# Kernel optimization log

Measured on AMD Instinct MI355X. Metric: run time of the kernel, lower is better.

The kernel has to match this reference:

```python
import jax, jax.numpy as jnp
import numpy as np

N_NODES = 50000
N_EDGES = 1600000
D_FEAT = 32
SCALE = 1.0
EPS = 1e-12


def setup_inputs() -> dict:
    key = jax.random.key(0)
    k1, k2 = jax.random.split(key)
    x = jax.random.normal(k1, (N_NODES, D_FEAT), dtype=jnp.float32)
    edge_index = jax.random.randint(k2, (2, N_EDGES), 0, N_NODES, dtype=jnp.int32)
    return {"x": x, "edge_index": edge_index}


def reference(x, edge_index):
    index_i = edge_index[0]  # target nodes (segments)
    index_j = edge_index[1]  # source nodes (gathered)

    # in-degree per target node, clamped to 1 (torch_scatter 'mean' semantics:
    # empty segments get mean 0)
    ones = jnp.ones((index_i.shape[0],), dtype=x.dtype)
    deg = jax.ops.segment_sum(ones, index_i, num_segments=N_NODES)
    deg = jnp.maximum(deg, 1.0)[:, None]  # [N, 1]

    # neighborhood mean of features
    mean = jax.ops.segment_sum(x[index_j], index_i, num_segments=N_NODES) / deg

    # neighborhood mean of squared deviations -> std
    reduced_x = (x - mean) ** 2
    var = jax.ops.segment_sum(reduced_x[index_j], index_i, num_segments=N_NODES) / deg
    std = jnp.sqrt(var + EPS)

    out = SCALE * x / std
    # replace infs with the original x, as in the torch module
    out = jnp.where(jnp.isinf(out), x, out)
    return out
```

## Files before the change

### kernel.cpp

```cpp
#include <hip/hip_runtime.h>
#include <hip/hip_fp16.h>
#include <math.h>

#define DF 32
#define EPSF 1e-12f
#define PB 128
#define PB_SHIFT 7
#define NBMAX 512
#define CAP 5120
#define CHUNK 4096
#define EPT 16

__global__ __launch_bounds__(256) void k_passA(
    const int* __restrict__ ii, const int* __restrict__ jj,
    const float* __restrict__ x, int* __restrict__ gcount,
    unsigned int* __restrict__ bucketed, __half* __restrict__ xh,
    int ne, int nb, int nfeat) {
  __shared__ int hist[NBMAX];
  __shared__ int histc[NBMAX];
  __shared__ int bb[NBMAX];
  __shared__ int excl_s[NBMAX];
  __shared__ int sc[256];
  __shared__ unsigned int stage[CHUNK];
  int t = threadIdx.x;
  hist[t] = 0; hist[t + 256] = 0;
  __syncthreads();

  int base = blockIdx.x * CHUNK;
  unsigned int pk[EPT];
  int rk[EPT];
#pragma unroll
  for (int k = 0; k < EPT; ++k) {
    int e = base + t + k * 256;
    if (e < ne) {
      int i = ii[e], j = jj[e];
      int b = i >> PB_SHIFT;
      pk[k] = ((unsigned)b << 23) | ((unsigned)(i & (PB - 1)) << 16) | (unsigned)j;
      rk[k] = atomicAdd(&hist[b], 1);
    } else {
      rk[k] = -1;
    }
  }

  {
    int base8 = blockIdx.x * (CHUNK / 8);
#pragma unroll
    for (int r = 0; r < 2; ++r) {
      int p8 = base8 + r * 256 + t;
      if (p8 * 8 < nfeat) {
        float4 a = ((const float4*)x)[2 * p8];
        float4 bq = ((const float4*)x)[2 * p8 + 1];
        union { __half2 h[4]; float4 f; } u;
        u.h[0] = __floats2half2_rn(a.x, a.y);
        u.h[1] = __floats2half2_rn(a.z, a.w);
        u.h[2] = __floats2half2_rn(bq.x, bq.y);
        u.h[3] = __floats2half2_rn(bq.z, bq.w);
        ((float4*)xh)[p8] = u.f;
      }
    }
  }
  __syncthreads();
  histc[t] = hist[t]; histc[t + 256] = hist[t + 256];
  __syncthreads();
#pragma unroll
  for (int b = t; b < NBMAX; b += 256) {
    int c = histc[b];
    bb[b] = (b < nb && c > 0) ? atomicAdd(&gcount[b], c) : 0;
  }
  int a0 = histc[2 * t], a1 = histc[2 * t + 1];
  sc[t] = a0 + a1;
  __syncthreads();
  int pv = sc[t];
  for (int s = 1; s < 256; s <<= 1) {
    int v = 0;
    if (t >= s) v = sc[t - s];
    __syncthreads();
    if (t >= s) sc[t] += v;
    __syncthreads();
  }
  int eP = sc[t] - pv;
  excl_s[2 * t] = eP;
  excl_s[2 * t + 1] = eP + a0;
  __syncthreads();
#pragma unroll
  for (int k = 0; k < EPT; ++k) {
    if (rk[k] >= 0) {
      int b = pk[k] >> 23;
      stage[excl_s[b] + rk[k]] = pk[k];
    }
  }
  __syncthreads();
  int bcnt = ne - base;
  if (bcnt > CHUNK) bcnt = CHUNK;
  for (int p = t; p < bcnt; p += 256) {
    unsigned int v = stage[p];
    int b = v >> 23;
    bucketed[(size_t)b * CAP + bb[b] + (p - excl_s[b])] = v;
  }
}

__global__ __launch_bounds__(256) void k_passB(
    const unsigned int* __restrict__ bucketed, const int* __restrict__ gcount,
    int* __restrict__ sortedj, int* __restrict__ deg_g, int* __restrict__ curend_g,
    int* __restrict__ perm, int n_nodes, int nb) {
  __shared__ int sc[256];
  __shared__ int lh[PB];
  __shared__ int lcur[PB];
  __shared__ int dh[PB];
  __shared__ int dcur[PB];
  __shared__ int sgbase;
  int b = blockIdx.x;
  int t = threadIdx.x;

  int g0 = (2 * t < nb) ? gcount[2 * t] : 0;
  int g1 = (2 * t + 1 < nb) ? gcount[2 * t + 1] : 0;
  sc[t] = g0 + g1;
  __syncthreads();
  int pv = sc[t];
  for (int s = 1; s < 256; s <<= 1) {
    int v = 0;
    if (t >= s) v = sc[t - s];
    __syncthreads();
    if (t >= s) sc[t] += v;
    __syncthreads();
  }
  if (2 * t == b) sgbase = sc[t] - pv;
  if (2 * t + 1 == b) sgbase = sc[t] - pv + g0;
  if (t < PB) { lh[t] = 0; dh[t] = 0; }
  __syncthreads();
  int gbase = sgbase;
  int cnt = gcount[b];

  const unsigned int* src = bucketed + (size_t)b * CAP;
  for (int p = t; p < cnt; p += 256) {
    int il = (src[p] >> 16) & (PB - 1);
    atomicAdd(&lh[il], 1);
  }
  __syncthreads();
  int a = (t < PB) ? lh[t] : 0;
  if (t < PB) sc[t] = a;
  __syncthreads();
  for (int s = 1; s < PB; s <<= 1) {
    int v = 0;
    if (t < PB && t >= s) v = sc[t - s];
    __syncthreads();
    if (t < PB && t >= s) sc[t] += v;
    __syncthreads();
  }
  int excl = (t < PB) ? sc[t] - a : 0;
  int node = b * PB + t;
  bool nvalid = (t < PB) && (node < n_nodes);
  if (t < PB) lcur[t] = excl;
  if (nvalid) {
    deg_g[node] = a;
    curend_g[node] = gbase + excl + a;
    atomicAdd(&dh[a < PB - 1 ? a : PB - 1], 1);
  }
  __syncthreads();
  int d0 = (t < PB) ? dh[t] : 0;
  if (t < PB) sc[t] = d0;
  __syncthreads();
  for (int s = 1; s < PB; s <<= 1) {
    int v = 0;
    if (t < PB && t >= s) v = sc[t - s];
    __syncthreads();
    if (t < PB && t >= s) sc[t] += v;
    __syncthreads();
  }
  if (t < PB) dcur[t] = sc[t] - d0;
  __syncthreads();
  if (nvalid) {
    int bin = a < PB - 1 ? a : PB - 1;
    int pos = atomicAdd(&dcur[bin], 1);
    perm[b * PB + pos] = node;
  } else if (t < PB) {
    perm[b * PB + t] = -1;
  }
  __syncthreads();
  for (int p = t; p < cnt; p += 256) {
    unsigned int v = src[p];
    int il = (v >> 16) & (PB - 1);
    int pos = atomicAdd(&lcur[il], 1);
    sortedj[gbase + pos] = (int)(v & 0xFFFFu);
  }
}

__global__ __launch_bounds__(256) void k_meansq(
    const int* __restrict__ perm, const int* __restrict__ sortedj,
    const int* __restrict__ curend, const int* __restrict__ deg,
    const __half* __restrict__ xh, const float* __restrict__ x,
    __half* __restrict__ yh, int n) {
  int wv = (int)((blockIdx.x * blockDim.x + threadIdx.x) >> 6);
  int lane = threadIdx.x & 63;
  int g = lane >> 2;
  int c = lane & 3;
  int ni = wv * 16 + g;
  int w = perm[ni];
  bool valid = (w >= 0);
  int dg = valid ? deg[w] : 0;
  int end = valid ? curend[w] : 0;
  int start = end - dg;
  int co = c * 8;
  __half2 aA0 = {}, aA1 = {}, aA2 = {}, aA3 = {};
  __half2 aB0 = {}, aB1 = {}, aB2 = {}, aB3 = {};
  int s = start;
  for (; s + 4 <= end; s += 4) {
    int j0 = sortedj[s], j1 = sortedj[s + 1], j2 = sortedj[s + 2], j3 = sortedj[s + 3];
    float4 v0 = *(const float4*)&xh[j0 * DF + co];
    float4 v1 = *(const float4*)&xh[j1 * DF + co];
    float4 v2 = *(const float4*)&xh[j2 * DF + co];
    float4 v3 = *(const float4*)&xh[j3 * DF + co];
    const __half2* h0 = (const __half2*)&v0;
    const __half2* h1 = (const __half2*)&v1;
    const __half2* h2 = (const __half2*)&v2;
    const __half2* h3 = (const __half2*)&v3;
    aA0 = __hadd2(aA0, h0[0]); aA1 = __hadd2(aA1, h0[1]);
    aA2 = __hadd2(aA2, h0[2]); aA3 = __hadd2(aA3, h0[3]);
    aB0 = __hadd2(aB0, h1[0]); aB1 = __hadd2(aB1, h1[1]);
    aB2 = __hadd2(aB2, h1[2]); aB3 = __hadd2(aB3, h1[3]);
    aA0 = __hadd2(aA0, h2[0]); aA1 = __hadd2(aA1, h2[1]);
    aA2 = __hadd2(aA2, h2[2]); aA3 = __hadd2(aA3, h2[3]);
    aB0 = __hadd2(aB0, h3[0]); aB1 = __hadd2(aB1, h3[1]);
    aB2 = __hadd2(aB2, h3[2]); aB3 = __hadd2(aB3, h3[3]);
  }
  for (; s < end; ++s) {
    int j = sortedj[s];
    float4 v = *(const float4*)&xh[j * DF + co];
    const __half2* h = (const __half2*)&v;
    aA0 = __hadd2(aA0, h[0]); aA1 = __hadd2(aA1, h[1]);
    aA2 = __hadd2(aA2, h[2]); aA3 = __hadd2(aA3, h[3]);
  }
  if (valid) {
    __half2 s0 = __hadd2(aA0, aB0), s1 = __hadd2(aA1, aB1);
    __half2 s2 = __hadd2(aA2, aB2), s3 = __hadd2(aA3, aB3);
    float inv = 1.0f / fmaxf((float)dg, 1.0f);
    float2 m0 = __half22float2(s0);
    float2 m1 = __half22float2(s1);
    float2 m2 = __half22float2(s2);
    float2 m3 = __half22float2(s3);
    float4 xa = *(const float4*)&x[w * DF + co];
    float4 xb = *(const float4*)&x[w * DF + co + 4];
    float d0 = xa.x - m0.x * inv;
    float d1 = xa.y - m0.y * inv;
    float d2 = xa.z - m1.x * inv;
    float d3 = xa.w - m1.y * inv;
    float d4 = xb.x - m2.x * inv;
    float d5 = xb.y - m2.y * inv;
    float d6 = xb.z - m3.x * inv;
    float d7 = xb.w - m3.y * inv;
    union { __half2 h[4]; float4 f; } u;
    u.h[0] = __floats2half2_rn(d0 * d0, d1 * d1);
    u.h[1] = __floats2half2_rn(d2 * d2, d3 * d3);
    u.h[2] = __floats2half2_rn(d4 * d4, d5 * d5);
    u.h[3] = __floats2half2_rn(d6 * d6, d7 * d7);
    *(float4*)&yh[w * DF + co] = u.f;
  }
}

__global__ __launch_bounds__(256) void k_varfinal(
    const int* __restrict__ perm, const int* __restrict__ sortedj,
    const int* __restrict__ curend, const int* __restrict__ deg,
    const __half* __restrict__ yh, const float* __restrict__ x,
    float* __restrict__ out, int n) {
  int wv = (int)((blockIdx.x * blockDim.x + threadIdx.x) >> 6);
  int lane = threadIdx.x & 63;
  int g = lane >> 2;
  int c = lane & 3;
  int ni = wv * 16 + g;
  int w = perm[ni];
  bool valid = (w >= 0);
  int dg = valid ? deg[w] : 0;
  int end = valid ? curend[w] : 0;
  int start = end - dg;
  int co = c * 8;
  float accA[8], accB[8];
#pragma unroll
  for (int k = 0; k < 8; ++k) { accA[k] = 0.f; accB[k] = 0.f; }
  int s = start;
  for (; s + 4 <= end; s += 4) {
    int j0 = sortedj[s], j1 = sortedj[s + 1], j2 = sortedj[s + 2], j3 = sortedj[s + 3];
    float4 v0 = *(const float4*)&yh[j0 * DF + co];
    float4 v1 = *(const float4*)&yh[j1 * DF + co];
    float4 v2 = *(const float4*)&yh[j2 * DF + co];
    float4 v3 = *(const float4*)&yh[j3 * DF + co];
    const __half2* h0 = (const __half2*)&v0;
    const __half2* h1 = (const __half2*)&v1;
    const __half2* h2 = (const __half2*)&v2;
    const __half2* h3 = (const __half2*)&v3;
#pragma unroll
    for (int k = 0; k < 4; ++k) {
      float2 f0 = __half22float2(h0[k]);
      float2 f1 = __half22float2(h1[k]);
      float2 f2 = __half22float2(h2[k]);
      float2 f3 = __half22float2(h3[k]);
      accA[2 * k]     += f0.x + f2.x;
      accA[2 * k + 1] += f0.y + f2.y;
      accB[2 * k]     += f1.x + f3.x;
      accB[2 * k + 1] += f1.y + f3.y;
    }
  }
  for (; s < end; ++s) {
    int j = sortedj[s];
    float4 v = *(const float4*)&yh[j * DF + co];
    const __half2* h = (const __half2*)&v;
#pragma unroll
    for (int k = 0; k < 4; ++k) {
      float2 f = __half22float2(h[k]);
      accA[2 * k]     += f.x;
      accA[2 * k + 1] += f.y;
    }
  }
  if (valid) {
    float dgc = fmaxf((float)dg, 1.0f);
    float4 xa = *(const float4*)&x[w * DF + co];
    float4 xb = *(const float4*)&x[w * DF + co + 4];
    float xs[8] = {xa.x, xa.y, xa.z, xa.w, xb.x, xb.y, xb.z, xb.w};
    float o[8];
#pragma unroll
    for (int k = 0; k < 8; ++k) {
      float sq = sqrtf((accA[k] + accB[k]) / dgc + EPSF);
      o[k] = xs[k] / sq;
      if (isinf(o[k])) o[k] = xs[k];
    }
    float4 oa = {o[0], o[1], o[2], o[3]};
    float4 ob = {o[4], o[5], o[6], o[7]};
    *(float4*)&out[w * DF + co] = oa;
    *(float4*)&out[w * DF + co + 4] = ob;
  }
}

extern "C" void kernel_launch(void* const* d_in, const int* in_sizes, int n_in,
                              void* d_out, int out_size, void* d_ws, size_t ws_size,
                              hipStream_t stream) {
  const float* x = (const float*)d_in[0];
  const int* ei = (const int*)d_in[1];
  const int n_nodes = in_sizes[0] / DF;
  const int ne = in_sizes[1] / 2;
  const int* ii = ei;
  const int* jj = ei + ne;
  const int nb = (n_nodes + PB - 1) / PB;
  const int nfeat = n_nodes * DF;
  const int nperm = nb * PB;

  char* wsb = (char*)d_ws;
  size_t off = 0;
  auto align16 = [](size_t v) { return (v + 15) & ~(size_t)15; };
  int* gcount = (int*)(wsb + off); off = align16(off + NBMAX * 4);
  int* deg    = (int*)(wsb + off); off = align16(off + (size_t)n_nodes * 4);
  int* curend = (int*)(wsb + off); off = align16(off + (size_t)n_nodes * 4);
  int* perm   = (int*)(wsb + off); off = align16(off + (size_t)nperm * 4);
  int* sortedj= (int*)(wsb + off); off = align16(off + (size_t)ne * 4);
  unsigned int* bucketed = (unsigned int*)(wsb + off);
  off = align16(off + (size_t)nb * CAP * 4);
  __half* xh = (__half*)(wsb + off); off = align16(off + (size_t)nfeat * 2);
  __half* yh = (__half*)(wsb + off);

  float* out = (float*)d_out;

  hipMemsetAsync(gcount, 0, NBMAX * sizeof(int), stream);

  int nblkA = (ne + CHUNK - 1) / CHUNK;
  int nblkF = (nfeat + CHUNK - 1) / CHUNK;
  if (nblkF > nblkA) nblkA = nblkF;
  k_passA<<<nblkA, 256, 0, stream>>>(ii, jj, x, gcount, bucketed, xh, ne, nb, nfeat);
  k_passB<<<nb, 256, 0, stream>>>(bucketed, gcount, sortedj, deg, curend, perm, n_nodes, nb);

  int gblocks = nperm / 64;
  k_meansq<<<gblocks, 256, 0, stream>>>(perm, sortedj, curend, deg, xh, x, yh, n_nodes);
  k_varfinal<<<gblocks, 256, 0, stream>>>(perm, sortedj, curend, deg, yh, x, out, n_nodes);
}
```

Before: 86.91 us.

## Fuse four kernels into one cooperative persistent kernel with grid syncs

Replaces the four separate launches (bucket, sort, mean, variance) with a single cooperative kernel of 512 blocks that separates the phases with grid-wide syncs. The fp16 conversion of x now runs on blocks that are idle during bucketing rather than being folded into the bucketing blocks. The gather loops become grid-stride loops unrolled to 8 neighbours. This removes per-launch overhead and inter-kernel gaps, at the cost of grid.sync latency, a fixed grid size, and fewer resident waves for the gather phases.

Result: slower. 288.4 us (+231.9%).

```diff
diff --git a/kernel.cpp b/kernel.cpp
--- a/kernel.cpp
+++ b/kernel.cpp
@@ -1,6 +1,9 @@
 #include <hip/hip_runtime.h>
+#include <hip/hip_cooperative_groups.h>
 #include <hip/hip_fp16.h>
 #include <math.h>
+
+namespace cg = cooperative_groups;
 
 #define DF 32
 #define EPSF 1e-12f
@@ -10,322 +13,319 @@
 #define CAP 5120
 #define CHUNK 4096
 #define EPT 16
-
-__global__ __launch_bounds__(256) void k_passA(
+#define GRID 512
+
+__global__ __launch_bounds__(256) void k_fused(
     const int* __restrict__ ii, const int* __restrict__ jj,
     const float* __restrict__ x, int* __restrict__ gcount,
     unsigned int* __restrict__ bucketed, __half* __restrict__ xh,
-    int ne, int nb, int nfeat) {
+    __half* __restrict__ yh, int* __restrict__ sortedj,
+    int* __restrict__ deg_g, int* __restrict__ curend_g,
+    int* __restrict__ perm, float* __restrict__ out,
+    int ne, int n_nodes, int nb, int nfeat) {
+  cg::grid_group grid = cg::this_grid();
   __shared__ int hist[NBMAX];
   __shared__ int histc[NBMAX];
   __shared__ int bb[NBMAX];
   __shared__ int excl_s[NBMAX];
   __shared__ int sc[256];
   __shared__ unsigned int stage[CHUNK];
-  int t = threadIdx.x;
-  hist[t] = 0; hist[t + 256] = 0;
-  __syncthreads();
-
-  int base = blockIdx.x * CHUNK;
-  unsigned int pk[EPT];
-  int rk[EPT];
-#pragma unroll
-  for (int k = 0; k < EPT; ++k) {
-    int e = base + t + k * 256;
-    if (e < ne) {
-      int i = ii[e], j = jj[e];
-      int b = i >> PB_SHIFT;
-      pk[k] = ((unsigned)b << 23) | ((unsigned)(i & (PB - 1)) << 16) | (unsigned)j;
-      rk[k] = atomicAdd(&hist[b], 1);
-    } else {
-      rk[k] = -1;
+  __shared__ int sgbase;
+  const int t = threadIdx.x;
+  const int bid = blockIdx.x;
+  const int nbA = (ne + CHUNK - 1) / CHUNK;
+
+  if (bid < nbA) {
+    hist[t] = 0; hist[t + 256] = 0;
+    __syncthreads();
+    int base = bid * CHUNK;
+    unsigned int pk[EPT];
+    int rk[EPT];
+#pragma unroll
+    for (int k = 0; k < EPT; ++k) {
+      int e = base + t + k * 256;
+      if (e < ne) {
+        int i = ii[e], j = jj[e];
+        int b = i >> PB_SHIFT;
+        pk[k] = ((unsigned)b << 23) | ((unsigned)(i & (PB - 1)) << 16) | (unsigned)j;
+        rk[k] = atomicAdd(&hist[b], 1);
+      } else {
+        rk[k] = -1;
+      }
+    }
+    __syncthreads();
+    histc[t] = hist[t]; histc[t + 256] = hist[t + 256];
+    __syncthreads();
+#pragma unroll
+    for (int b = t; b < NBMAX; b += 256) {
+      int c = histc[b];
+      bb[b] = (b < nb && c > 0) ? atomicAdd(&gcount[b], c) : 0;
+    }
+    int a0 = histc[2 * t], a1 = histc[2 * t + 1];
+    sc[t] = a0 + a1;
+    __syncthreads();
+    int pv = sc[t];
+    for (int s = 1; s < 256; s <<= 1) {
+      int v = 0;
+      if (t >= s) v = sc[t - s];
+      __syncthreads();
+      if (t >= s) sc[t] += v;
+      __syncthreads();
+    }
+    int eP = sc[t] - pv;
+    excl_s[2 * t] = eP;
+    excl_s[2 * t + 1] = eP + a0;
+    __syncthreads();
+#pragma unroll
+    for (int k = 0; k < EPT; ++k) {
+      if (rk[k] >= 0) {
+        int b = pk[k] >> 23;
+        stage[excl_s[b] + rk[k]] = pk[k];
+      }
+    }
+    __syncthreads();
+    int bcnt = ne - base;
+    if (bcnt > CHUNK) bcnt = CHUNK;
+    for (int p = t; p < bcnt; p += 256) {
+      unsigned int v = stage[p];
+      int b = v >> 23;
+      bucketed[(size_t)b * CAP + bb[b] + (p - excl_s[b])] = v;
+    }
+  } else {
+    int n8 = nfeat >> 3;
+    int nconv = (int)gridDim.x - nbA;
+    for (int p8 = (bid - nbA) * 256 + t; p8 < n8; p8 += nconv * 256) {
+      float4 a = ((const float4*)x)[2 * p8];
+      float4 bq = ((const float4*)x)[2 * p8 + 1];
+      union { __half2 h[4]; float4 f; } u;
+      u.h[0] = __floats2half2_rn(a.x, a.y);
+      u.h[1] = __floats2half2_rn(a.z, a.w);
+      u.h[2] = __floats2half2_rn(bq.x, bq.y);
+      u.h[3] = __floats2half2_rn(bq.z, bq.w);
+      ((float4*)xh)[p8] = u.f;
     }
   }
-
-  {
-    int base8 = blockIdx.x * (CHUNK / 8);
-#pragma unroll
-    for (int r = 0; r < 2; ++r) {
-      int p8 = base8 + r * 256 + t;
-      if (p8 * 8 < nfeat) {
-        float4 a = ((const float4*)x)[2 * p8];
-        float4 bq = ((const float4*)x)[2 * p8 + 1];
-        union { __half2 h[4]; float4 f; } u;
-        u.h[0] = __floats2half2_rn(a.x, a.y);
-        u.h[1] = __floats2half2_rn(a.z, a.w);
-        u.h[2] = __floats2half2_rn(bq.x, bq.y);
-        u.h[3] = __floats2half2_rn(bq.z, bq.w);
-        ((float4*)xh)[p8] = u.f;
-      }
+  grid.sync();
+
+  if (bid < nb) {
+    int* lh = hist; int* lcur = histc; int* dh = bb; int* dcur = excl_s;
+    int g0 = (2 * t < nb) ? gcount[2 * t] : 0;
+    int g1 = (2 * t + 1 < nb) ? gcount[2 * t + 1] : 0;
+    sc[t] = g0 + g1;
+    __syncthreads();
+    int pv = sc[t];
+    for (int s = 1; s < 256; s <<= 1) {
+      int v = 0;
+      if (t >= s) v = sc[t - s];
+      __syncthreads();
+      if (t >= s) sc[t] += v;
+      __syncthreads();
+    }
+    if (2 * t == bid) sgbase = sc[t] - pv;
+    if (2 * t + 1 == bid) sgbase = sc[t] - pv + g0;
+    if (t < PB) { lh[t] = 0; dh[t] = 0; }
+    __syncthreads();
+    int gbase = sgbase;
+    int cnt = gcount[bid];
+    const unsigned int* src = bucketed + (size_t)bid * CAP;
+    for (int p = t; p < cnt; p += 256) {
+      int il = (src[p] >> 16) & (PB - 1);
+      atomicAdd(&lh[il], 1);
+    }
+    __syncthreads();
+    int a = (t < PB) ? lh[t] : 0;
+    if (t < PB) sc[t] = a;
+    __syncthreads();
+    for (int s = 1; s < PB; s <<= 1) {
+      int v = 0;
+      if (t < PB && t >= s) v = sc[t - s];
+      __syncthreads();
+      if (t < PB && t >= s) sc[t] += v;
+      __syncthreads();
+    }
+    int excl = (t < PB) ? sc[t] - a : 0;
+    int node = bid * PB + t;
+    bool nvalid = (t < PB) && (node < n_nodes);
+    if (t < PB) lcur[t] = excl;
+    if (nvalid) {
+      deg_g[node] = a;
+      curend_g[node] = gbase + excl + a;
+      atomicAdd(&dh[a < PB - 1 ? a : PB - 1], 1);
+    }
+    __syncthreads();
+    int d0 = (t < PB) ? dh[t] : 0;
+    if (t < PB) sc[t] = d0;
+    __syncthreads();
+    for (int s = 1; s < PB; s <<= 1) {
+      int v = 0;
+      if (t < PB && t >= s) v = sc[t - s];
+      __syncthreads();
+      if (t < PB && t >= s) sc[t] += v;
+      __syncthreads();
+    }
+    if (t < PB) dcur[t] = sc[t] - d0;
+    __syncthreads();
+    if (nvalid) {
+      int bin = a < PB - 1 ? a : PB - 1;
+      int pos = atomicAdd(&dcur[bin], 1);
+      perm[bid * PB + pos] = node;
+    } else if (t < PB) {
+      perm[bid * PB + t] = -1;
+    }
+    __syncthreads();
+    for (int p = t; p < cnt; p += 256) {
+      unsigned int v = src[p];
+      int il = (v >> 16) & (PB - 1);
+      int pos = atomicAdd(&lcur[il], 1);
+      sortedj[gbase + pos] = (int)(v & 0xFFFFu);
     }
   }
-  __syncthreads();
-  histc[t] = hist[t]; histc[t + 256] = hist[t + 256];
-  __syncthreads();
-#pragma unroll
-  for (int b = t; b < NBMAX; b += 256) {
-    int c = histc[b];
-    bb[b] = (b < nb && c > 0) ? atomicAdd(&gcount[b], c) : 0;
+  grid.sync();
+
+  const int nperm = nb * PB;
+  const int totslots = (int)gridDim.x * 4 * 16;
+  const int lane = t & 63;
+  const int g = lane >> 2;
+  const int c = lane & 3;
+  const int co = c * 8;
+  int wv0 = ((bid * 256 + t) >> 6) * 16 + g;
+  for (int ni = wv0; ni < nperm; ni += totslots) {
+    int w = perm[ni];
+    bool valid = (w >= 0);
+    int dg = valid ? deg_g[w] : 0;
+    int end = valid ? curend_g[w] : 0;
+    int start = end - dg;
+    __half2 aA0 = {}, aA1 = {}, aA2 = {}, aA3 = {};
+    __half2 aB0 = {}, aB1 = {}, aB2 = {}, aB3 = {};
+    int s = start;
+    for (; s + 8 <= end; s += 8) {
+      int j0 = sortedj[s],     j1 = sortedj[s + 1], j2 = sortedj[s + 2], j3 = sortedj[s + 3];
+      int j4 = sortedj[s + 4], j5 = sortedj[s + 5], j6 = sortedj[s + 6], j7 = sortedj[s + 7];
+      float4 v0 = *(const float4*)&xh[j0 * DF + co];
+      float4 v1 = *(const float4*)&xh[j1 * DF + co];
+      float4 v2 = *(const float4*)&xh[j2 * DF + co];
+      float4 v3 = *(const float4*)&xh[j3 * DF + co];
+      float4 v4 = *(const float4*)&xh[j4 * DF + co];
+      float4 v5 = *(const float4*)&xh[j5 * DF + co];
+      float4 v6 = *(const float4*)&xh[j6 * DF + co];
+      float4 v7 = *(const float4*)&xh[j7 * DF + co];
+      const __half2* h0 = (const __half2*)&v0; const __half2* h1 = (const __half2*)&v1;
+      const __half2* h2 = (const __half2*)&v2; const __half2* h3 = (const __half2*)&v3;
+      const __half2* h4 = (const __half2*)&v4; const __half2* h5 = (const __half2*)&v5;
+      const __half2* h6 = (const __half2*)&v6; const __half2* h7 = (const __half2*)&v7;
+      aA0 = __hadd2(aA0, h0[0]); aA1 = __hadd2(aA1, h0[1]); aA2 = __hadd2(aA2, h0[2]); aA3 = __hadd2(aA3, h0[3]);
+      aB0 = __hadd2(aB0, h1[0]); aB1 = __hadd2(aB1, h1[1]); aB2 = __hadd2(aB2, h1[2]); aB3 = __hadd2(aB3, h1[3]);
+      aA0 = __hadd2(aA0, h2[0]); aA1 = __hadd2(aA1, h2[1]); aA2 = __hadd2(aA2, h2[2]); aA3 = __hadd2(aA3, h2[3]);
+      aB0 = __hadd2(aB0, h3[0]); aB1 = __hadd2(aB1, h3[1]); aB2 = __hadd2(aB2, h3[2]); aB3 = __hadd2(aB3, h3[3]);
+      aA0 = __hadd2(aA0, h4[0]); aA1 = __hadd2(aA1, h4[1]); aA2 = __hadd2(aA2, h4[2]); aA3 = __hadd2(aA3, h4[3]);
+      aB0 = __hadd2(aB0, h5[0]); aB1 = __hadd2(aB1, h5[1]); aB2 = __hadd2(aB2, h5[2]); aB3 = __hadd2(aB3, h5[3]);
+      aA0 = __hadd2(aA0, h6[0]); aA1 = __hadd2(aA1, h6[1]); aA2 = __hadd2(aA2, h6[2]); aA3 = __hadd2(aA3, h6[3]);
+      aB0 = __hadd2(aB0, h7[0]); aB1 = __hadd2(aB1, h7[1]); aB2 = __hadd2(aB2, h7[2]); aB3 = __hadd2(aB3, h7[3]);
+    }
+    for (; s < end; ++s) {
+      int j = sortedj[s];
+      float4 v = *(const float4*)&xh[j * DF + co];
+      const __half2* h = (const __half2*)&v;
+      aA0 = __hadd2(aA0, h[0]); aA1 = __hadd2(aA1, h[1]);
+      aA2 = __hadd2(aA2, h[2]); aA3 = __hadd2(aA3, h[3]);
+    }
+    if (valid) {
+      __half2 s0 = __hadd2(aA0, aB0), s1 = __hadd2(aA1, aB1);
+      __half2 s2 = __hadd2(aA2, aB2), s3 = __hadd2(aA3, aB3);
+      float inv = 1.0f / fmaxf((float)dg, 1.0f);
+      float2 m0 = __half22float2(s0);
+      float2 m1 = __half22float2(s1);
+      float2 m2 = __half22float2(s2);
+      float2 m3 = __half22float2(s3);
+      float4 xa = *(const float4*)&x[w * DF + co];
+      float4 xb = *(const float4*)&x[w * DF + co + 4];
+      float d0 = xa.x - m0.x * inv;
+      float d1 = xa.y - m0.y * inv;
+      float d2 = xa.z - m1.x * inv;
+      float d3 = xa.w - m1.y * inv;
+      float d4 = xb.x - m2.x * inv;
+      float d5 = xb.y - m2.y * inv;
+      float d6 = xb.z - m3.x * inv;
+      float d7 = xb.w - m3.y * inv;
+      union { __half2 h[4]; float4 f; } u;
+      u.h[0] = __floats2half2_rn(d0 * d0, d1 * d1);
+      u.h[1] = __floats2half2_rn(d2 * d2, d3 * d3);
+      u.h[2] = __floats2half2_rn(d4 * d4, d5 * d5);
+      u.h[3] = __floats2half2_rn(d6 * d6, d7 * d7);
+      *(float4*)&yh[w * DF + co] = u.f;
+    }
   }
-  int a0 = histc[2 * t], a1 = histc[2 * t + 1];
-  sc[t] = a0 + a1;
-  __syncthreads();
-  int pv = sc[t];
-  for (int s = 1; s < 256; s <<= 1) {
-    int v = 0;
-    if (t >= s) v = sc[t - s];
-    __syncthreads();
-    if (t >= s) sc[t] += v;
-    __syncthreads();
-  }
-  int eP = sc[t] - pv;
-  excl_s[2 * t] = eP;
-  excl_s[2 * t + 1] = eP + a0;
-  __syncthreads();
-#pragma unroll
-  for (int k = 0; k < EPT; ++k) {
-    if (rk[k] >= 0) {
-      int b = pk[k] >> 23;
-      stage[excl_s[b] + rk[k]] = pk[k];
-    }
-  }
-  __syncthreads();
-  int bcnt = ne - base;
-  if (bcnt > CHUNK) bcnt = CHUNK;
-  for (int p = t; p < bcnt; p += 256) {
-    unsigned int v = stage[p];
-    int b = v >> 23;
-    bucketed[(size_t)b * CAP + bb[b] + (p - excl_s[b])] = v;
-  }
-}
-
-__global__ __launch_bounds__(256) void k_passB(
-    const unsigned int* __restrict__ bucketed, const int* __restrict__ gcount,
-    int* __restrict__ sortedj, int* __restrict__ deg_g, int* __restrict__ curend_g,
-    int* __restrict__ perm, int n_nodes, int nb) {
-  __shared__ int sc[256];
-  __shared__ int lh[PB];
-  __shared__ int lcur[PB];
-  __shared__ int dh[PB];
-  __shared__ int dcur[PB];
-  __shared__ int sgbase;
-  int b = blockIdx.x;
-  int t = threadIdx.x;
-
-  int g0 = (2 * t < nb) ? gcount[2 * t] : 0;
-  int g1 = (2 * t + 1 < nb) ? gcount[2 * t + 1] : 0;
-  sc[t] = g0 + g1;
-  __syncthreads();
-  int pv = sc[t];
-  for (int s = 1; s < 256; s <<= 1) {
-    int v = 0;
-    if (t >= s) v = sc[t - s];
-    __syncthreads();
-    if (t >= s) sc[t] += v;
-    __syncthreads();
-  }
-  if (2 * t == b) sgbase = sc[t] - pv;
-  if (2 * t + 1 == b) sgbase = sc[t] - pv + g0;
-  if (t < PB) { lh[t] = 0; dh[t] = 0; }
-  __syncthreads();
-  int gbase = sgbase;
-  int cnt = gcount[b];
-
-  const unsigned int* src = bucketed + (size_t)b * CAP;
-  for (int p = t; p < cnt; p += 256) {
-    int il = (src[p] >> 16) & (PB - 1);
-    atomicAdd(&lh[il], 1);
-  }
-  __syncthreads();
-  int a = (t < PB) ? lh[t] : 0;
-  if (t < PB) sc[t] = a;
-  __syncthreads();
-  for (int s = 1; s < PB; s <<= 1) {
-    int v = 0;
-    if (t < PB && t >= s) v = sc[t - s];
-    __syncthreads();
-    if (t < PB && t >= s) sc[t] += v;
-    __syncthreads();
-  }
-  int excl = (t < PB) ? sc[t] - a : 0;
-  int node = b * PB + t;
-  bool nvalid = (t < PB) && (node < n_nodes);
-  if (t < PB) lcur[t] = excl;
-  if (nvalid) {
-    deg_g[node] = a;
-    curend_g[node] = gbase + excl + a;
-    atomicAdd(&dh[a < PB - 1 ? a : PB - 1], 1);
-  }
-  __syncthreads();
-  int d0 = (t < PB) ? dh[t] : 0;
-  if (t < PB) sc[t] = d0;
-  __syncthreads();
-  for (int s = 1; s < PB; s <<= 1) {
-    int v = 0;
-    if (t < PB && t >= s) v = sc[t - s];
-    __syncthreads();
-    if (t < PB && t >= s) sc[t] += v;
-    __syncthreads();
-  }
-  if (t < PB) dcur[t] = sc[t] - d0;
-  __syncthreads();
-  if (nvalid) {
-    int bin = a < PB - 1 ? a : PB - 1;
-    int pos = atomicAdd(&dcur[bin], 1);
-    perm[b * PB + pos] = node;
-  } else if (t < PB) {
-    perm[b * PB + t] = -1;
-  }
-  __syncthreads();
-  for (int p = t; p < cnt; p += 256) {
-    unsigned int v = src[p];
-    int il = (v >> 16) & (PB - 1);
-    int pos = atomicAdd(&lcur[il], 1);
-    sortedj[gbase + pos] = (int)(v & 0xFFFFu);
-  }
-}
-
-__global__ __launch_bounds__(256) void k_meansq(
-    const int* __restrict__ perm, const int* __restrict__ sortedj,
-    const int* __restrict__ curend, const int* __restrict__ deg,
-    const __half* __restrict__ xh, const float* __restrict__ x,
-    __half* __restrict__ yh, int n) {
-  int wv = (int)((blockIdx.x * blockDim.x + threadIdx.x) >> 6);
-  int lane = threadIdx.x & 63;
-  int g = lane >> 2;
-  int c = lane & 3;
-  int ni = wv * 16 + g;
-  int w = perm[ni];
-  bool valid = (w >= 0);
-  int dg = valid ? deg[w] : 0;
-  int end = valid ? curend[w] : 0;
-  int start = end - dg;
-  int co = c * 8;
-  __half2 aA0 = {}, aA1 = {}, aA2 = {}, aA3 = {};
-  __half2 aB0 = {}, aB1 = {}, aB2 = {}, aB3 = {};
-  int s = start;
-  for (; s + 4 <= end; s += 4) {
-    int j0 = sortedj[s], j1 = sortedj[s + 1], j2 = sortedj[s + 2], j3 = sortedj[s + 3];
-    float4 v0 = *(const float4*)&xh[j0 * DF + co];
-    float4 v1 = *(const float4*)&xh[j1 * DF + co];
-    float4 v2 = *(const float4*)&xh[j2 * DF + co];
-    float4 v3 = *(const float4*)&xh[j3 * DF + co];
-    const __half2* h0 = (const __half2*)&v0;
-    const __half2* h1 = (const __half2*)&v1;
-    const __half2* h2 = (const __half2*)&v2;
-    const __half2* h3 = (const __half2*)&v3;
-    aA0 = __hadd2(aA0, h0[0]); aA1 = __hadd2(aA1, h0[1]);
-    aA2 = __hadd2(aA2, h0[2]); aA3 = __hadd2(aA3, h0[3]);
-    aB0 = __hadd2(aB0, h1[0]); aB1 = __hadd2(aB1, h1[1]);
-    aB2 = __hadd2(aB2, h1[2]); aB3 = __hadd2(aB3, h1[3]);
-    aA0 = __hadd2(aA0, h2[0]); aA1 = __hadd2(aA1, h2[1]);
-    aA2 = __hadd2(aA2, h2[2]); aA3 = __hadd2(aA3, h2[3]);
-    aB0 = __hadd2(aB0, h3[0]); aB1 = __hadd2(aB1, h3[1]);
-    aB2 = __hadd2(aB2, h3[2]); aB3 = __hadd2(aB3, h3[3]);
-  }
-  for (; s < end; ++s) {
-    int j = sortedj[s];
-    float4 v = *(const float4*)&xh[j * DF + co];
-    const __half2* h = (const __half2*)&v;
-    aA0 = __hadd2(aA0, h[0]); aA1 = __hadd2(aA1, h[1]);
-    aA2 = __hadd2(aA2, h[2]); aA3 = __hadd2(aA3, h[3]);
-  }
-  if (valid) {
-    __half2 s0 = __hadd2(aA0, aB0), s1 = __hadd2(aA1, aB1);
-    __half2 s2 = __hadd2(aA2, aB2), s3 = __hadd2(aA3, aB3);
-    float inv = 1.0f / fmaxf((float)dg, 1.0f);
-    float2 m0 = __half22float2(s0);
-    float2 m1 = __half22float2(s1);
-    float2 m2 = __half22float2(s2);
-    float2 m3 = __half22float2(s3);
-    float4 xa = *(const float4*)&x[w * DF + co];
-    float4 xb = *(const float4*)&x[w * DF + co + 4];
-    float d0 = xa.x - m0.x * inv;
-    float d1 = xa.y - m0.y * inv;
-    float d2 = xa.z - m1.x * inv;
-    float d3 = xa.w - m1.y * inv;
-    float d4 = xb.x - m2.x * inv;
-    float d5 = xb.y - m2.y * inv;
-    float d6 = xb.z - m3.x * inv;
-    float d7 = xb.w - m3.y * inv;
-    union { __half2 h[4]; float4 f; } u;
-    u.h[0] = __floats2half2_rn(d0 * d0, d1 * d1);
-    u.h[1] = __floats2half2_rn(d2 * d2, d3 * d3);
-    u.h[2] = __floats2half2_rn(d4 * d4, d5 * d5);
-    u.h[3] = __floats2half2_rn(d6 * d6, d7 * d7);
-    *(float4*)&yh[w * DF + co] = u.f;
-  }
-}
-
-__global__ __launch_bounds__(256) void k_varfinal(
-    const int* __restrict__ perm, const int* __restrict__ sortedj,
-    const int* __restrict__ curend, const int* __restrict__ deg,
-    const __half* __restrict__ yh, const float* __restrict__ x,
-    float* __restrict__ out, int n) {
-  int wv = (int)((blockIdx.x * blockDim.x + threadIdx.x) >> 6);
-  int lane = threadIdx.x & 63;
-  int g = lane >> 2;
-  int c = lane & 3;
-  int ni = wv * 16 + g;
-  int w = perm[ni];
-  bool valid = (w >= 0);
-  int dg = valid ? deg[w] : 0;
-  int end = valid ? curend[w] : 0;
-  int start = end - dg;
-  int co = c * 8;
-  float accA[8], accB[8];
-#pragma unroll
-  for (int k = 0; k < 8; ++k) { accA[k] = 0.f; accB[k] = 0.f; }
-  int s = start;
-  for (; s + 4 <= end; s += 4) {
-    int j0 = sortedj[s], j1 = sortedj[s + 1], j2 = sortedj[s + 2], j3 = sortedj[s + 3];
-    float4 v0 = *(const float4*)&yh[j0 * DF + co];
-    float4 v1 = *(const float4*)&yh[j1 * DF + co];
-    float4 v2 = *(const float4*)&yh[j2 * DF + co];
-    float4 v3 = *(const float4*)&yh[j3 * DF + co];
-    const __half2* h0 = (const __half2*)&v0;
-    const __half2* h1 = (const __half2*)&v1;
-    const __half2* h2 = (const __half2*)&v2;
-    const __half2* h3 = (const __half2*)&v3;
-#pragma unroll
-    for (int k = 0; k < 4; ++k) {
-      float2 f0 = __half22float2(h0[k]);
-      float2 f1 = __half22float2(h1[k]);
-      float2 f2 = __half22float2(h2[k]);
-      float2 f3 = __half22float2(h3[k]);
-      accA[2 * k]     += f0.x + f2.x;
-      accA[2 * k + 1] += f0.y + f2.y;
-      accB[2 * k]     += f1.x + f3.x;
-      accB[2 * k + 1] += f1.y + f3.y;
-    }
-  }
-  for (; s < end; ++s) {
-    int j = sortedj[s];
-    float4 v = *(const float4*)&yh[j * DF + co];
-    const __half2* h = (const __half2*)&v;
-#pragma unroll
-    for (int k = 0; k < 4; ++k) {
-      float2 f = __half22float2(h[k]);
-      accA[2 * k]     += f.x;
-      accA[2 * k + 1] += f.y;
-    }
-  }
-  if (valid) {
-    float dgc = fmaxf((float)dg, 1.0f);
-    float4 xa = *(const float4*)&x[w * DF + co];
-    float4 xb = *(const float4*)&x[w * DF + co + 4];
-    float xs[8] = {xa.x, xa.y, xa.z, xa.w, xb.x, xb.y, xb.z, xb.w};
-    float o[8];
-#pragma unroll
-    for (int k = 0; k < 8; ++k) {
-      float sq = sqrtf((accA[k] + accB[k]) / dgc + EPSF);
-      o[k] = xs[k] / sq;
-      if (isinf(o[k])) o[k] = xs[k];
-    }
-    float4 oa = {o[0], o[1], o[2], o[3]};
-    float4 ob = {o[4], o[5], o[6], o[7]};
-    *(float4*)&out[w * DF + co] = oa;
-    *(float4*)&out[w * DF + co + 4] = ob;
+  grid.sync();
+
+  for (int ni = wv0; ni < nperm; ni += totslots) {
+    int w = perm[ni];
+    bool valid = (w >= 0);
+    int dg = valid ? deg_g[w] : 0;
+    int end = valid ? curend_g[w] : 0;
+    int start = end - dg;
+    float accA[8], accB[8];
+#pragma unroll
+    for (int k = 0; k < 8; ++k) { accA[k] = 0.f; accB[k] = 0.f; }
+    int s = start;
+    for (; s + 8 <= end; s += 8) {
+      int j0 = sortedj[s],     j1 = sortedj[s + 1], j2 = sortedj[s + 2], j3 = sortedj[s + 3];
+      int j4 = sortedj[s + 4], j5 = sortedj[s + 5], j6 = sortedj[s + 6], j7 = sortedj[s + 7];
+      float4 v0 = *(const float4*)&yh[j0 * DF + co];
+      float4 v1 = *(const float4*)&yh[j1 * DF + co];
+      float4 v2 = *(const float4*)&yh[j2 * DF + co];
+      float4 v3 = *(const float4*)&yh[j3 * DF + co];
+      float4 v4 = *(const float4*)&yh[j4 * DF + co];
+      float4 v5 = *(const float4*)&yh[j5 * DF + co];
+      float4 v6 = *(const float4*)&yh[j6 * DF + co];
+      float4 v7 = *(const float4*)&yh[j7 * DF + co];
+      const __half2* h0 = (const __half2*)&v0; const __half2* h1 = (const __half2*)&v1;
+      const __half2* h2 = (const __half2*)&v2; const __half2* h3 = (const __half2*)&v3;
+      const __half2* h4 = (const __half2*)&v4; const __half2* h5 = (const __half2*)&v5;
+      const __half2* h6 = (const __half2*)&v6; const __half2* h7 = (const __half2*)&v7;
+#pragma unroll
+      for (int k = 0; k < 4; ++k) {
+        float2 f0 = __half22float2(h0[k]);
+        float2 f1 = __half22float2(h1[k]);
+        float2 f2 = __half22float2(h2[k]);
+        float2 f3 = __half22float2(h3[k]);
+        float2 f4 = __half22float2(h4[k]);
+        float2 f5 = __half22float2(h5[k]);
+        float2 f6 = __half22float2(h6[k]);
+        float2 f7 = __half22float2(h7[k]);
+        accA[2 * k]     += (f0.x + f2.x) + (f4.x + f6.x);
+        accA[2 * k + 1] += (f0.y + f2.y) + (f4.y + f6.y);
+        accB[2 * k]     += (f1.x + f3.x) + (f5.x + f7.x);
+        accB[2 * k + 1] += (f1.y + f3.y) + (f5.y + f7.y);
+      }
+    }
+    for (; s < end; ++s) {
+      int j = sortedj[s];
+      float4 v = *(const float4*)&yh[j * DF + co];
+      const __half2* h = (const __half2*)&v;
+#pragma unroll
+      for (int k = 0; k < 4; ++k) {
+        float2 f = __half22float2(h[k]);
+        accA[2 * k]     += f.x;
+        accA[2 * k + 1] += f.y;
+      }
+    }
+    if (valid) {
+      float dgc = fmaxf((float)dg, 1.0f);
+      float4 xa = *(const float4*)&x[w * DF + co];
+      float4 xb = *(const float4*)&x[w * DF + co + 4];
+      float xs[8] = {xa.x, xa.y, xa.z, xa.w, xb.x, xb.y, xb.z, xb.w};
+      float o[8];
+#pragma unroll
+      for (int k = 0; k < 8; ++k) {
+        float sq = sqrtf((accA[k] + accB[k]) / dgc + EPSF);
+        o[k] = xs[k] / sq;
+        if (isinf(o[k])) o[k] = xs[k];
+      }
+      float4 oa = {o[0], o[1], o[2], o[3]};
+      float4 ob = {o[4], o[5], o[6], o[7]};
+      *(float4*)&out[w * DF + co] = oa;
+      *(float4*)&out[w * DF + co + 4] = ob;
+    }
   }
 }
 
@@ -334,13 +334,13 @@
                               hipStream_t stream) {
   const float* x = (const float*)d_in[0];
   const int* ei = (const int*)d_in[1];
-  const int n_nodes = in_sizes[0] / DF;
-  const int ne = in_sizes[1] / 2;
+  int n_nodes = in_sizes[0] / DF;
+  int ne = in_sizes[1] / 2;
   const int* ii = ei;
   const int* jj = ei + ne;
-  const int nb = (n_nodes + PB - 1) / PB;
-  const int nfeat = n_nodes * DF;
-  const int nperm = nb * PB;
+  int nb = (n_nodes + PB - 1) / PB;
+  int nfeat = n_nodes * DF;
+  int nperm = nb * PB;
 
   char* wsb = (char*)d_ws;
   size_t off = 0;
@@ -359,13 +359,12 @@
 
   hipMemsetAsync(gcount, 0, NBMAX * sizeof(int), stream);
 
-  int nblkA = (ne + CHUNK - 1) / CHUNK;
-  int nblkF = (nfeat + CHUNK - 1) / CHUNK;
-  if (nblkF > nblkA) nblkA = nblkF;
-  k_passA<<<nblkA, 256, 0, stream>>>(ii, jj, x, gcount, bucketed, xh, ne, nb, nfeat);
-  k_passB<<<nb, 256, 0, stream>>>(bucketed, gcount, sortedj, deg, curend, perm, n_nodes, nb);
-
-  int gblocks = nperm / 64;
-  k_meansq<<<gblocks, 256, 0, stream>>>(perm, sortedj, curend, deg, xh, x, yh, n_nodes);
-  k_varfinal<<<gblocks, 256, 0, stream>>>(perm, sortedj, curend, deg, yh, x, out, n_nodes);
+  void* args[] = {
+    (void*)&ii, (void*)&jj, (void*)&x, (void*)&gcount, (void*)&bucketed,
+    (void*)&xh, (void*)&yh, (void*)&sortedj, (void*)&deg, (void*)&curend,
+    (void*)&perm, (void*)&out, (void*)&ne, (void*)&n_nodes, (void*)&nb,
+    (void*)&nfeat
+  };
+  hipLaunchCooperativeKernel((const void*)k_fused, dim3(GRID), dim3(256),
+                             args, 0, stream);
 }
```
